# Kernel tuning notes

Hardware: AMD Instinct MI355X
Metric: run time of the kernel (lower is better)

Reference implementation:

```python
import jax, jax.numpy as jnp
import numpy as np

N, M_CODES, Z_DIM = 4096, 4096, 1024


def setup_inputs() -> dict:
    key = jax.random.key(0)
    k1, k2 = jax.random.split(key)
    z = jax.random.normal(k1, (N, Z_DIM), dtype=jnp.float32)
    e = jax.random.normal(k2, (M_CODES, Z_DIM), dtype=jnp.float32)
    return {"z": z, "e": e}


def reference(z, e):
    # Squared pairwise L2 distances [N, M] via GEMM expansion:
    # ||z_i - e_j||^2 = ||z_i||^2 + ||e_j||^2 - 2 z_i . e_j
    z_sq = jnp.sum(z * z, axis=1)               # [N]
    e_sq = jnp.sum(e * e, axis=1)               # [M]
    cross = jnp.einsum('nd,md->nm', z, e)       # [N, M]
    dist = z_sq[:, None] + e_sq[None, :] - 2.0 * cross  # [N, M]
    # min over dim 0 (over data points N) -> per-code nearest distance [M]
    loss = jnp.mean(jnp.min(dist, axis=0))
    return loss
```

## Files before the change

kernel.cpp:

```cpp
#include <hip/hip_runtime.h>
#include <hip/hip_bf16.h>
#include <stdint.h>

#define N_PTS   4096
#define M_CODES 4096
#define ZDIM    1024
#define KG      (ZDIM / 8)

typedef __attribute__((ext_vector_type(8))) short bf16x8;
typedef __attribute__((ext_vector_type(4))) float f32x4;

__device__ __forceinline__ unsigned short f2bf(float f) {
    __hip_bfloat16 h = __float2bfloat16(f);
    return *reinterpret_cast<unsigned short*>(&h);
}
__device__ __forceinline__ unsigned enc_f32(float f) {
    unsigned u = __float_as_uint(f);
    return (u & 0x80000000u) ? ~u : (u | 0x80000000u);
}
__device__ __forceinline__ float dec_f32(unsigned e) {
    unsigned u = (e & 0x80000000u) ? (e ^ 0x80000000u) : ~u;
    return __uint_as_float(u);
}

#define PREP_PITCH 1032
__global__ __launch_bounds__(256) void prep_kernel(
    const float* __restrict__ z, const float* __restrict__ e,
    unsigned short* __restrict__ zb, unsigned short* __restrict__ eb,
    float* __restrict__ zsq, float* __restrict__ esq,
    unsigned* __restrict__ min_enc) {
    __shared__ unsigned short tile[16 * PREP_PITCH];
    __shared__ float redbuf[4 * 16];

    const int t = threadIdx.x;
    const int b = blockIdx.x;
    if (b < 16) min_enc[b * 256 + t] = 0xFFFFFFFFu;

    const bool is_z = b < 256;
    const int rb = b & 255;
    const float* src = (is_z ? z : e) + (size_t)rb * 16 * ZDIM;
    unsigned short* dst = (is_z ? zb : eb) + (size_t)rb * 16384;
    const int w = t >> 6, lane = t & 63;

    #pragma unroll
    for (int it = 0; it < 16; it++) {
        float4 v = reinterpret_cast<const float4*>(src + (size_t)it * ZDIM)[t];
        ushort4 o;
        o.x = f2bf(v.x); o.y = f2bf(v.y); o.z = f2bf(v.z); o.w = f2bf(v.w);
        *reinterpret_cast<ushort4*>(&tile[it * PREP_PITCH + t * 4]) = o;
    }
    __syncthreads();

    float s = 0.f;
    #pragma unroll
    for (int it2 = 0; it2 < 8; it2++) {
        const int c = it2 * 256 + t;
        const int kg = c >> 4, r16 = c & 15;
        bf16x8 val = *reinterpret_cast<const bf16x8*>(
            &tile[r16 * PREP_PITCH + kg * 8]);
        *reinterpret_cast<bf16x8*>(&dst[(size_t)c * 8]) = val;
        #pragma unroll
        for (int j = 0; j < 8; j++) {
            float f = __uint_as_float(((unsigned)(unsigned short)val[j]) << 16);
            s = fmaf(f, f, s);
        }
    }
    s += __shfl_xor(s, 16, 64);
    s += __shfl_xor(s, 32, 64);
    if (lane < 16) redbuf[w * 16 + lane] = s;
    __syncthreads();
    if (t < 16) {
        float sq = redbuf[t] + redbuf[16 + t] + redbuf[32 + t] + redbuf[48 + t];
        const int row = rb * 16 + t;
        if (is_z) zsq[row] = sq; else esq[row] = sq;
    }
}

__global__ __launch_bounds__(256, 4) void gemm_min_kernel(
    const unsigned short* __restrict__ zb, const unsigned short* __restrict__ eb,
    const float* __restrict__ zsq, unsigned* __restrict__ min_enc) {
    __shared__ float zsq_s[128];
    __shared__ float colmin[2][128];

    const int t = threadIdx.x;
    const int bx = blockIdx.x;
    const int by = blockIdx.y;
    const int lane = t & 63;
    const int w = t >> 6;
    const int wm = w >> 1, wn = w & 1;
    const int lrow = lane & 15;
    const int q = lane >> 4;

    if (t < 128) zsq_s[t] = zsq[by * 128 + t];

    f32x4 acc[4][4];
    #pragma unroll
    for (int i = 0; i < 4; i++)
        #pragma unroll
        for (int j = 0; j < 4; j++) acc[i][j] = (f32x4){0.f, 0.f, 0.f, 0.f};

    const unsigned short* a_base =
        zb + (size_t)(by * 8 + wm * 4) * 16384 + lane * 8;
    const unsigned short* b_base =
        eb + (size_t)(bx * 8 + wn * 4) * 16384 + lane * 8;

    for (int kg0 = 0; kg0 < KG; kg0 += 8) {
        #pragma unroll
        for (int s = 0; s < 2; s++) {
            const int off = kg0 * 128 + s * 512;
            bf16x8 a[4], bb[4];
            #pragma unroll
            for (int am = 0; am < 4; am++)
                a[am] = *(const bf16x8*)(a_base + (size_t)am * 16384 + off);
            #pragma unroll
            for (int an = 0; an < 4; an++)
                bb[an] = *(const bf16x8*)(b_base + (size_t)an * 16384 + off);
            #pragma unroll
            for (int am = 0; am < 4; am++)
                #pragma unroll
                for (int an = 0; an < 4; an++)
                    acc[am][an] = __builtin_amdgcn_mfma_f32_16x16x32_bf16(
                        a[am], bb[an], acc[am][an], 0, 0, 0);
        }
    }

    __syncthreads();

    #pragma unroll
    for (int an = 0; an < 4; an++) {
        float v = 3.4e38f;
        #pragma unroll
        for (int am = 0; am < 4; am++) {
            const int rbase = wm * 64 + am * 16 + q * 4;
            f32x4 c = acc[am][an];
            v = fminf(v, zsq_s[rbase + 0] - 2.f * c[0]);
            v = fminf(v, zsq_s[rbase + 1] - 2.f * c[1]);
            v = fminf(v, zsq_s[rbase + 2] - 2.f * c[2]);
            v = fminf(v, zsq_s[rbase + 3] - 2.f * c[3]);
        }
        v = fminf(v, __shfl_xor(v, 16, 64));
        v = fminf(v, __shfl_xor(v, 32, 64));
        if (q == 0) colmin[wm][wn * 64 + an * 16 + lrow] = v;
    }
    __syncthreads();
    if (t < 128) {
        const float m = fminf(colmin[0][t], colmin[1][t]);
        atomicMin(&min_enc[bx * 128 + t], enc_f32(m));
    }
}

__global__ __launch_bounds__(256) void finalize_kernel(
    const unsigned* __restrict__ min_enc, const float* __restrict__ esq,
    float* __restrict__ out) {
    const int t = threadIdx.x;
    float s = 0.f;
    #pragma unroll
    for (int i = 0; i < M_CODES / 256; i++) {
        const int j = i * 256 + t;
        s += dec_f32(min_enc[j]) + esq[j];
    }
    #pragma unroll
    for (int off = 1; off < 64; off <<= 1) s += __shfl_xor(s, off, 64);
    __shared__ float red[4];
    if ((t & 63) == 0) red[t >> 6] = s;
    __syncthreads();
    if (t == 0) out[0] = (red[0] + red[1] + red[2] + red[3]) * (1.f / M_CODES);
}

extern "C" void kernel_launch(void* const* d_in, const int* in_sizes, int n_in,
                              void* d_out, int out_size, void* d_ws, size_t ws_size,
                              hipStream_t stream) {
    (void)in_sizes; (void)n_in; (void)out_size; (void)ws_size;
    const float* z = (const float*)d_in[0];
    const float* e = (const float*)d_in[1];
    char* ws = (char*)d_ws;
    unsigned short* zb = (unsigned short*)ws;
    unsigned short* eb = (unsigned short*)(ws + ((size_t)8 << 20));
    float* zsq = (float*)(ws + ((size_t)16 << 20));
    float* esq = (float*)(ws + ((size_t)16 << 20) + 16384);
    unsigned* min_enc = (unsigned*)(ws + ((size_t)16 << 20) + 32768);

    prep_kernel<<<dim3(512), dim3(256), 0, stream>>>(
        z, e, zb, eb, zsq, esq, min_enc);
    gemm_min_kernel<<<dim3(32, 32), dim3(256), 0, stream>>>(
        zb, eb, zsq, min_enc);
    finalize_kernel<<<dim3(1), dim3(256), 0, stream>>>(min_enc, esq, (float*)d_out);
}
```

Before: 118.4 us.

## Stage A operand in LDS via double-buffered async global-to-LDS loads

The z (A) operand is now staged into a double-buffered shared-memory tile using global_load_lds, and the next K stage is prefetched while the current one is consumed. B is still read directly from global. The aim is to halve redundant global reads of A, which are shared by the two column warps, and to overlap its loads with MFMA work. In exchange it adds 32KB of LDS per block and a barrier every stage, and it relies on the barrier waiting for the async loads to finish.

```diff
diff --git a/kernel.cpp b/kernel.cpp
--- a/kernel.cpp
+++ b/kernel.cpp
@@ -79,6 +79,7 @@
 __global__ __launch_bounds__(256, 4) void gemm_min_kernel(
     const unsigned short* __restrict__ zb, const unsigned short* __restrict__ eb,
     const float* __restrict__ zsq, unsigned* __restrict__ min_enc) {
+    __shared__ __align__(16) unsigned short As[16384];
     __shared__ float zsq_s[128];
     __shared__ float colmin[2][128];
 
@@ -99,22 +100,46 @@
         #pragma unroll
         for (int j = 0; j < 4; j++) acc[i][j] = (f32x4){0.f, 0.f, 0.f, 0.f};
 
-    const unsigned short* a_base =
-        zb + (size_t)(by * 8 + wm * 4) * 16384 + lane * 8;
+    const int seg_half = t >> 7;
+    const int inner = (t & 127) * 8;
+    const int lds_w = w * 512;
+    const size_t a_seg0 = (size_t)(by * 8) * 16384;
+
     const unsigned short* b_base =
         eb + (size_t)(bx * 8 + wn * 4) * 16384 + lane * 8;
 
-    for (int kg0 = 0; kg0 < KG; kg0 += 8) {
+#define DMA_STAGE(st_)                                                        \
+    {                                                                         \
+        const int buf_ = ((st_) & 1) * 8192;                                  \
+        const int koff_ = (st_) * 1024;                                       \
+        _Pragma("unroll")                                                     \
+        for (int j = 0; j < 4; j++) {                                         \
+            const unsigned short* ga = zb + a_seg0 +                          \
+                (size_t)(j * 2 + seg_half) * 16384 + koff_ + inner;           \
+            __builtin_amdgcn_global_load_lds(                                 \
+                (const __attribute__((address_space(1))) void*)ga,            \
+                (__attribute__((address_space(3))) void*)(As + buf_ +         \
+                    j * 2048 + lds_w), 16, 0, 0);                             \
+        }                                                                     \
+    }
+
+    DMA_STAGE(0);
+    for (int st = 0; st < 16; st++) {
+        __syncthreads();
+        if (st < 15) DMA_STAGE(st + 1);
+        const int buf = (st & 1) * 8192;
+        const int koff = st * 1024;
         #pragma unroll
         for (int s = 0; s < 2; s++) {
-            const int off = kg0 * 128 + s * 512;
             bf16x8 a[4], bb[4];
             #pragma unroll
+            for (int an = 0; an < 4; an++)
+                bb[an] = *(const bf16x8*)(b_base + (size_t)an * 16384 +
+                                          koff + s * 512);
+            #pragma unroll
             for (int am = 0; am < 4; am++)
-                a[am] = *(const bf16x8*)(a_base + (size_t)am * 16384 + off);
-            #pragma unroll
-            for (int an = 0; an < 4; an++)
-                bb[an] = *(const bf16x8*)(b_base + (size_t)an * 16384 + off);
+                a[am] = *(const bf16x8*)(As + buf + (wm * 4 + am) * 1024 +
+                                         s * 512 + lane * 8);
             #pragma unroll
             for (int am = 0; am < 4; am++)
                 #pragma unroll
@@ -123,6 +148,7 @@
                         a[am], bb[an], acc[am][an], 0, 0, 0);
         }
     }
+#undef DMA_STAGE
 
     __syncthreads();
 
```

Result: faster. 112.5 us (-4.9%).
